# Performance work log

Hardware: AMD Instinct MI355X
Metric: run time of the kernel (lower is better)

The kernel has to match this reference:

```python
import jax, jax.numpy as jnp
import numpy as np

BIT_W = 8   # config.bit_wt
BIT_A = 8   # config.bit_act (activations sliced 2 bits at a time)
STRIDE = (1, 1)
PAD = 1


def _conv(a, w):
    # NCHW input, OIHW weight, stride 1, symmetric padding 1 (matches wrapped Conv2d)
    return jax.lax.conv_general_dilated(
        a, w, window_strides=STRIDE, padding=[(PAD, PAD), (PAD, PAD)],
        dimension_numbers=("NCHW", "OIHW", "NCHW"))


def setup_inputs() -> dict:
    key = jax.random.key(0)
    k1, k2, k3 = jax.random.split(key, 3)
    x = jax.random.normal(k1, (64, 64, 56, 56), dtype=jnp.float32)
    weight = jax.random.normal(k2, (64, 64, 3, 3), dtype=jnp.float32)
    bias = jax.random.normal(k3, (64,), dtype=jnp.float32)
    scale_a = jnp.full((1,), 20.0, dtype=jnp.float32)      # conv_q.scale
    scale_w = jnp.full((1,), 20.0, dtype=jnp.float32)      # wrapped_module.weight_scale
    zero_point = jnp.full((1,), -128.0, dtype=jnp.float32)  # conv_q.zero_point
    return {"x": x, "weight": weight, "bias": bias,
            "scale_a": scale_a, "scale_w": scale_w, "zero_point": zero_point}


def reference(x, weight, bias, scale_a, scale_w, zero_point):
    sa = scale_a[0]
    sw = scale_w[0]
    zp = zero_point[0]
    # activation quantization: round(x*scale_a - zero_point), clamp to [0, 2^bit_act - 1]
    q_in = jnp.clip(jnp.round(x * sa - zp), 0.0, 2.0 ** BIT_A - 1.0)
    # weight quantization: round(w * scale_w), interpreted in two's complement
    q_w = jnp.round(weight * sw)
    w_off = q_w + 2.0 ** BIT_W  # (w + (1 << bit_weight)) before bit masking

    acc = jnp.zeros((), dtype=jnp.float32)
    for ba in range(BIT_A // 2):
        # 2-bit activation slice: (a >> 2*ba) & 3
        a_sl = jnp.mod(jnp.floor(q_in / (4.0 ** ba)), 4.0)
        for bw in range(BIT_W):
            # weight bit bw: ((w + 2^B) >> bw) & 1
            w_bit = jnp.mod(jnp.floor(w_off / (2.0 ** bw)), 2.0)
            r = _conv(a_sl, w_bit)
            sgn = -1.0 if bw == BIT_W - 1 else 1.0  # MSB = sign bit (two's complement)
            acc = acc + sgn * (2.0 ** (2 * ba + bw)) * r

    # zero-point correction: conv(ones * zp, q_w) added back (no-op when zp == 0)
    acc = acc + zp * _conv(jnp.ones_like(q_in), q_w)

    out = acc / (sw * sa) + bias[None, :, None, None]
    return out
```

## Files before the change

### kernel.cpp

```cpp
#include <hip/hip_runtime.h>


typedef int v4i __attribute__((ext_vector_type(4)));
typedef float v4f __attribute__((ext_vector_type(4)));

__global__ __launch_bounds__(64) void prep_wq(const float* __restrict__ wt,
                                              const float* __restrict__ sw_p,
                                              const float* __restrict__ zp_p,
                                              signed char* __restrict__ w8,
                                              float* __restrict__ corr_tab) {
  const int o = blockIdx.x;
  const int i = threadIdx.x;
  const float sw = sw_p[0];
  const float* wp = wt + (size_t)(o * 64 + i) * 9;
  int q[9];
#pragma unroll
  for (int k = 0; k < 9; ++k) q[k] = (int)rintf(wp[k] * sw);
#pragma unroll
  for (int k = 0; k < 9; ++k)
    w8[(o * 9 + k) * 64 + i] = (signed char)(q[k] & 255);

  int stc[9], srw[9];
#pragma unroll
  for (int k = 0; k < 9; ++k) {
    int a = (int)(signed char)(q[k] & 255);
    int b = q[k];
#pragma unroll
    for (int off = 32; off; off >>= 1) {
      a += __shfl_xor(a, off);
      b += __shfl_xor(b, off);
    }
    stc[k] = a; srw[k] = b;
  }
  const float zp = zp_p[0];
  if (i < 9) {
    const int v = i / 3, hc = i % 3;
    float corr = 0.0f;
#pragma unroll
    for (int k = 0; k < 9; ++k) {
      const int kh = k / 3, kw = k % 3;
      const bool drop = (v == 1 && kh == 0) || (v == 2 && kh == 2) ||
                        (hc == 1 && kw == 0) || (hc == 2 && kw == 2);
      if (!drop) corr += 128.0f * (float)stc[k] + zp * (float)srw[k];
    }
    corr_tab[i * 64 + o] = corr;
  }
}

__global__ __launch_bounds__(256, 4) void conv_fused(
    const float* __restrict__ x, const signed char* __restrict__ w8,
    const float* __restrict__ corr_tab, const float* __restrict__ bias,
    const float* __restrict__ sa_p, const float* __restrict__ sw_p,
    const float* __restrict__ zp_p, float* __restrict__ out) {
  __shared__ __align__(16) signed char lds[22272];
  const int tid = threadIdx.x;
  const int b = blockIdx.x;
  const int g = (b & 7) * 112 + (b >> 3);
  const int n = (g * 2341) >> 15;
  const int h0 = (g - n * 14) * 4;
  const float sa = sa_p[0], zp = zp_p[0];
  const float* xim = x + (size_t)n * 200704;

#pragma unroll 2
  for (int it = 0; it < 6; ++it) {
    const int idx = tid + 256 * it;
    if (idx < 1344) {
      const int cg = idx & 15;
      const int rem = idx >> 4;
      const int row = (rem * 2341) >> 15;
      const int w4 = rem - row * 14;
      const int ih = h0 - 1 + row;
      const bool valid = (unsigned)ih < 56u;
      v4f v[4];
      if (valid) {
#pragma unroll
        for (int j = 0; j < 4; ++j)
          v[j] = *(const v4f*)(xim + (size_t)(cg * 4 + j) * 3136 + ih * 56 + w4 * 4);
      }
#pragma unroll
      for (int e = 0; e < 4; ++e) {
        int dw = 0;
        if (valid) {
#pragma unroll
          for (int j = 0; j < 4; ++j) {
            float tq;
            {
#pragma clang fp contract(off)
              tq = v[j][e] * sa - zp;
            }
            float qf = rintf(tq);
            qf = fminf(fmaxf(qf, 0.0f), 255.0f);
            const int bb = ((int)qf - 128) & 255;
            dw |= bb << (8 * j);
          }
        }
        const int c = w4 * 4 + 1 + e;
        const int t = (c >> 1) & 3;
        ((int*)lds)[(row * 58 + c) * 16 + (((cg >> 2) ^ t) << 2) + (cg & 3)] = dw;
      }
    } else {
      const int z = idx - 1344;
      const int loc = z >> 4, d = z & 15;
      const int row = loc >> 1, side = loc & 1;
      ((int*)lds)[(row * 58 + side * 57) * 16 + d] = 0;
    }
  }
  __syncthreads();

  const int lane = tid & 63;
  const int wv = tid >> 6;
  const int phalf = wv & 1;
  const int ogp = wv >> 1;
  const int ln = lane & 15;
  const int kg = lane >> 4;
  const int oa = ogp * 32 + ln;

  const signed char* wba = w8 + (size_t)oa * 576 + kg * 16;
  v4i Ba[9], Bb[9];
#pragma unroll
  for (int t = 0; t < 9; ++t) {
    Ba[t] = *(const v4i*)(wba + t * 64);
    Bb[t] = *(const v4i*)(wba + 9216 + t * 64);
  }

  const float sw = sw_p[0];
  const float rden = 1.0f / (sw * sa);
  const float boa = bias[oa], bob = bias[oa + 16];
  const float cFa = corr_tab[oa];
  const float cFb = corr_tab[oa + 16];
  float* const outa = out + (size_t)(n * 64 + oa) * 3136 + h0 * 56;
  float* const outb = outa + 16 * 3136;

#pragma unroll 1
  for (int t = 0; t < 7; ++t) {
    const int pb = phalf * 112 + t * 16;
    const int pa = pb + ln;
    const int hr = (pa * 9363) >> 19;
    const int wc = pa - hr * 56;
    int coff[3];
#pragma unroll
    for (int kw = 0; kw < 3; ++kw) {
      const int c = wc + kw;
      coff[kw] = c * 64 + ((kg ^ ((c >> 1) & 3)) << 4);
    }
    const signed char* rowb = lds + hr * 3712;
    v4i acca = {0, 0, 0, 0}, accb = {0, 0, 0, 0};
#pragma unroll
    for (int kh = 0; kh < 3; ++kh) {
#pragma unroll
      for (int kw = 0; kw < 3; ++kw) {
        const v4i A = *(const v4i*)(rowb + kh * 3712 + coff[kw]);
        acca = __builtin_amdgcn_mfma_i32_16x16x64_i8(A, Ba[kh * 3 + kw], acca, 0, 0, 0);
        accb = __builtin_amdgcn_mfma_i32_16x16x64_i8(A, Bb[kh * 3 + kw], accb, 0, 0, 0);
      }
    }
    const int pxb = pb + kg * 4;
    float ta[4], tb[4];
#pragma unroll
    for (int e = 0; e < 4; ++e) {
      const int px = pxb + e;
      const int hh = (px * 9363) >> 19;
      const int ww = px - hh * 56;
      const int hg = h0 + hh;
      float ca = cFa, cb = cFb;
      if ((hg == 0) | (hg == 55) | (ww == 0) | (ww == 55)) {
        const int vcase = (hg == 0) ? 1 : ((hg == 55) ? 2 : 0);
        const int hcase = (ww == 0) ? 1 : ((ww == 55) ? 2 : 0);
        const int cidx = (vcase * 3 + hcase) * 64;
        ca = corr_tab[cidx + oa];
        cb = corr_tab[cidx + oa + 16];
      }
      ta[e] = ((float)acca[e] + ca) * rden + boa;
      tb[e] = ((float)accb[e] + cb) * rden + bob;
    }
    *(float4*)(outa + pxb) = make_float4(ta[0], ta[1], ta[2], ta[3]);
    *(float4*)(outb + pxb) = make_float4(tb[0], tb[1], tb[2], tb[3]);
  }
}

extern "C" void kernel_launch(void* const* d_in, const int* in_sizes, int n_in,
                              void* d_out, int out_size, void* d_ws, size_t ws_size,
                              hipStream_t stream) {
  const float* x    = (const float*)d_in[0];
  const float* wt   = (const float*)d_in[1];
  const float* bias = (const float*)d_in[2];
  const float* sa   = (const float*)d_in[3];
  const float* sw   = (const float*)d_in[4];
  const float* zp   = (const float*)d_in[5];
  float* out = (float*)d_out;

  char* ws = (char*)d_ws;
  signed char* w8 = (signed char*)ws;
  float* corr_tab = (float*)(ws + 36864);

  prep_wq<<<64, 64, 0, stream>>>(wt, sw, zp, w8, corr_tab);
  conv_fused<<<896, 256, 0, stream>>>(x, w8, corr_tab, bias, sa, sw, zp, out);
}
```

Baseline: 131.4 us.

## Halve conv row tile to two rows and give each wave 16 channels

Each block now computes 2 output rows instead of 4, so the grid doubles to 1792 blocks and LDS shrinks to 14848 bytes. Each wave now owns 16 output channels across both rows rather than 32 channels over half the pixels, which halves the resident weight registers and MFMA accumulators. Launch bounds are raised to 8 blocks per SM. The aim is higher occupancy and a more even spread of blocks across CUs, at the cost of more halo rows re-read and quantized per output row.

```diff
diff --git a/kernel.cpp b/kernel.cpp
--- a/kernel.cpp
+++ b/kernel.cpp
@@ -47,24 +47,24 @@
   }
 }
 
-__global__ __launch_bounds__(256, 4) void conv_fused(
+__global__ __launch_bounds__(256, 8) void conv_fused(
     const float* __restrict__ x, const signed char* __restrict__ w8,
     const float* __restrict__ corr_tab, const float* __restrict__ bias,
     const float* __restrict__ sa_p, const float* __restrict__ sw_p,
     const float* __restrict__ zp_p, float* __restrict__ out) {
-  __shared__ __align__(16) signed char lds[22272];
+  __shared__ __align__(16) signed char lds[14848];
   const int tid = threadIdx.x;
   const int b = blockIdx.x;
-  const int g = (b & 7) * 112 + (b >> 3);
-  const int n = (g * 2341) >> 15;
-  const int h0 = (g - n * 14) * 4;
+  const int g = (b & 7) * 224 + (b >> 3);
+  const int n = (g * 2341) >> 16;
+  const int h0 = (g - n * 28) * 2;
   const float sa = sa_p[0], zp = zp_p[0];
   const float* xim = x + (size_t)n * 200704;
 
 #pragma unroll 2
-  for (int it = 0; it < 6; ++it) {
+  for (int it = 0; it < 4; ++it) {
     const int idx = tid + 256 * it;
-    if (idx < 1344) {
+    if (idx < 896) {
       const int cg = idx & 15;
       const int rem = idx >> 4;
       const int row = (rem * 2341) >> 15;
@@ -99,7 +99,7 @@
         ((int*)lds)[(row * 58 + c) * 16 + (((cg >> 2) ^ t) << 2) + (cg & 3)] = dw;
       }
     } else {
-      const int z = idx - 1344;
+      const int z = idx - 896;
       const int loc = z >> 4, d = z & 15;
       const int row = loc >> 1, side = loc & 1;
       ((int*)lds)[(row * 58 + side * 57) * 16 + d] = 0;
@@ -109,33 +109,26 @@
 
   const int lane = tid & 63;
   const int wv = tid >> 6;
-  const int phalf = wv & 1;
-  const int ogp = wv >> 1;
   const int ln = lane & 15;
   const int kg = lane >> 4;
-  const int oa = ogp * 32 + ln;
+  const int oa = wv * 16 + ln;
 
   const signed char* wba = w8 + (size_t)oa * 576 + kg * 16;
-  v4i Ba[9], Bb[9];
+  v4i Ba[9];
 #pragma unroll
-  for (int t = 0; t < 9; ++t) {
-    Ba[t] = *(const v4i*)(wba + t * 64);
-    Bb[t] = *(const v4i*)(wba + 9216 + t * 64);
-  }
+  for (int t = 0; t < 9; ++t) Ba[t] = *(const v4i*)(wba + t * 64);
 
   const float sw = sw_p[0];
   const float rden = 1.0f / (sw * sa);
-  const float boa = bias[oa], bob = bias[oa + 16];
+  const float boa = bias[oa];
   const float cFa = corr_tab[oa];
-  const float cFb = corr_tab[oa + 16];
   float* const outa = out + (size_t)(n * 64 + oa) * 3136 + h0 * 56;
-  float* const outb = outa + 16 * 3136;
 
 #pragma unroll 1
   for (int t = 0; t < 7; ++t) {
-    const int pb = phalf * 112 + t * 16;
+    const int pb = t * 16;
     const int pa = pb + ln;
-    const int hr = (pa * 9363) >> 19;
+    const int hr = pa >= 56;
     const int wc = pa - hr * 56;
     int coff[3];
 #pragma unroll
@@ -144,37 +137,32 @@
       coff[kw] = c * 64 + ((kg ^ ((c >> 1) & 3)) << 4);
     }
     const signed char* rowb = lds + hr * 3712;
-    v4i acca = {0, 0, 0, 0}, accb = {0, 0, 0, 0};
+    v4i acca = {0, 0, 0, 0};
 #pragma unroll
     for (int kh = 0; kh < 3; ++kh) {
 #pragma unroll
       for (int kw = 0; kw < 3; ++kw) {
         const v4i A = *(const v4i*)(rowb + kh * 3712 + coff[kw]);
         acca = __builtin_amdgcn_mfma_i32_16x16x64_i8(A, Ba[kh * 3 + kw], acca, 0, 0, 0);
-        accb = __builtin_amdgcn_mfma_i32_16x16x64_i8(A, Bb[kh * 3 + kw], accb, 0, 0, 0);
       }
     }
     const int pxb = pb + kg * 4;
-    float ta[4], tb[4];
+    float ta[4];
 #pragma unroll
     for (int e = 0; e < 4; ++e) {
       const int px = pxb + e;
-      const int hh = (px * 9363) >> 19;
+      const int hh = px >= 56;
       const int ww = px - hh * 56;
       const int hg = h0 + hh;
-      float ca = cFa, cb = cFb;
+      float ca = cFa;
       if ((hg == 0) | (hg == 55) | (ww == 0) | (ww == 55)) {
         const int vcase = (hg == 0) ? 1 : ((hg == 55) ? 2 : 0);
         const int hcase = (ww == 0) ? 1 : ((ww == 55) ? 2 : 0);
-        const int cidx = (vcase * 3 + hcase) * 64;
-        ca = corr_tab[cidx + oa];
-        cb = corr_tab[cidx + oa + 16];
+        ca = corr_tab[(vcase * 3 + hcase) * 64 + oa];
       }
       ta[e] = ((float)acca[e] + ca) * rden + boa;
-      tb[e] = ((float)accb[e] + cb) * rden + bob;
     }
     *(float4*)(outa + pxb) = make_float4(ta[0], ta[1], ta[2], ta[3]);
-    *(float4*)(outb + pxb) = make_float4(tb[0], tb[1], tb[2], tb[3]);
   }
 }
 
@@ -194,5 +182,5 @@
   float* corr_tab = (float*)(ws + 36864);
 
   prep_wq<<<64, 64, 0, stream>>>(wt, sw, zp, w8, corr_tab);
-  conv_fused<<<896, 256, 0, stream>>>(x, w8, corr_tab, bias, sa, sw, zp, out);
+  conv_fused<<<1792, 256, 0, stream>>>(x, w8, corr_tab, bias, sa, sw, zp, out);
 }
```

Result: slower. 138.3 us (+5.2%).

## Split activation quantization into a separate int8 pre-pass kernel

Applied to the files above, without the earlier changes.

Moves activation quantization out of the conv kernel into a standalone kernel that writes a padded, swizzled int8 activation image to workspace, including zeroed halo rows and columns. The conv kernel then just copies its tile of int8 rows into LDS and runs the MFMA loop. This removes redundant halo-row float loads and per-block quantization ALU work from the conv kernel. In exchange it adds an extra kernel launch and a round trip of the int8 tensor through global memory.

```diff
diff --git a/kernel.cpp b/kernel.cpp
--- a/kernel.cpp
+++ b/kernel.cpp
@@ -3,6 +3,9 @@
 
 typedef int v4i __attribute__((ext_vector_type(4)));
 typedef float v4f __attribute__((ext_vector_type(4)));
+
+#define QA_ROW 3712
+#define QA_IMG 215296
 
 __global__ __launch_bounds__(64) void prep_wq(const float* __restrict__ wt,
                                               const float* __restrict__ sw_p,
@@ -47,62 +50,81 @@
   }
 }
 
-__global__ __launch_bounds__(256, 4) void conv_fused(
-    const float* __restrict__ x, const signed char* __restrict__ w8,
+__global__ __launch_bounds__(256) void quant_a(const float* __restrict__ x,
+                                               const float* __restrict__ sa_p,
+                                               const float* __restrict__ zp_p,
+                                               signed char* __restrict__ qa) {
+  const int bx = blockIdx.x;
+  const int n = blockIdx.y;
+  const int tid = threadIdx.x;
+  const float sa = sa_p[0], zp = zp_p[0];
+  const float* xim = x + (size_t)n * 200704;
+  signed char* const qim = qa + (size_t)n * QA_IMG;
+
+#pragma unroll
+  for (int it = 0; it < 4; ++it) {
+    const int idx = tid + 256 * it;
+    if (idx < 896) {
+      const int cg = idx & 15;
+      const int rem = idx >> 4;
+      const int r = (rem * 2341) >> 15;
+      const int w4 = rem - r * 14;
+      const int ih = bx * 4 + r;
+      v4f v[4];
+#pragma unroll
+      for (int j = 0; j < 4; ++j)
+        v[j] = *(const v4f*)(xim + (size_t)(cg * 4 + j) * 3136 + ih * 56 + w4 * 4);
+#pragma unroll
+      for (int e = 0; e < 4; ++e) {
+        int dw = 0;
+#pragma unroll
+        for (int j = 0; j < 4; ++j) {
+          float tq;
+          {
+#pragma clang fp contract(off)
+            tq = v[j][e] * sa - zp;
+          }
+          float qf = rintf(tq);
+          qf = fminf(fmaxf(qf, 0.0f), 255.0f);
+          dw |= (((int)qf - 128) & 255) << (8 * j);
+        }
+        const int c = w4 * 4 + 1 + e;
+        const int t = (c >> 1) & 3;
+        *(int*)(qim + (ih + 1) * QA_ROW + c * 64 +
+                (((cg >> 2) ^ t) << 4) + ((cg & 3) << 2)) = dw;
+      }
+    } else {
+      const int z = idx - 896;
+      const int loc = z >> 4, d = z & 15;
+      const int r = loc >> 1, side = loc & 1;
+      *(int*)(qim + (bx * 4 + 1 + r) * QA_ROW + side * 57 * 64 + d * 4) = 0;
+    }
+  }
+  if (bx == 0 && tid < 232)
+    ((uint4*)qim)[tid] = make_uint4(0, 0, 0, 0);
+  if (bx == 13 && tid < 232)
+    ((uint4*)(qim + (size_t)57 * QA_ROW))[tid] = make_uint4(0, 0, 0, 0);
+}
+
+__global__ __launch_bounds__(256, 4) void conv_mfma(
+    const signed char* __restrict__ qa, const signed char* __restrict__ w8,
     const float* __restrict__ corr_tab, const float* __restrict__ bias,
     const float* __restrict__ sa_p, const float* __restrict__ sw_p,
-    const float* __restrict__ zp_p, float* __restrict__ out) {
+    float* __restrict__ out) {
   __shared__ __align__(16) signed char lds[22272];
   const int tid = threadIdx.x;
   const int b = blockIdx.x;
   const int g = (b & 7) * 112 + (b >> 3);
   const int n = (g * 2341) >> 15;
   const int h0 = (g - n * 14) * 4;
-  const float sa = sa_p[0], zp = zp_p[0];
-  const float* xim = x + (size_t)n * 200704;
-
-#pragma unroll 2
-  for (int it = 0; it < 6; ++it) {
-    const int idx = tid + 256 * it;
-    if (idx < 1344) {
-      const int cg = idx & 15;
-      const int rem = idx >> 4;
-      const int row = (rem * 2341) >> 15;
-      const int w4 = rem - row * 14;
-      const int ih = h0 - 1 + row;
-      const bool valid = (unsigned)ih < 56u;
-      v4f v[4];
-      if (valid) {
-#pragma unroll
-        for (int j = 0; j < 4; ++j)
-          v[j] = *(const v4f*)(xim + (size_t)(cg * 4 + j) * 3136 + ih * 56 + w4 * 4);
-      }
-#pragma unroll
-      for (int e = 0; e < 4; ++e) {
-        int dw = 0;
-        if (valid) {
-#pragma unroll
-          for (int j = 0; j < 4; ++j) {
-            float tq;
-            {
-#pragma clang fp contract(off)
-              tq = v[j][e] * sa - zp;
-            }
-            float qf = rintf(tq);
-            qf = fminf(fmaxf(qf, 0.0f), 255.0f);
-            const int bb = ((int)qf - 128) & 255;
-            dw |= bb << (8 * j);
-          }
-        }
-        const int c = w4 * 4 + 1 + e;
-        const int t = (c >> 1) & 3;
-        ((int*)lds)[(row * 58 + c) * 16 + (((cg >> 2) ^ t) << 2) + (cg & 3)] = dw;
-      }
-    } else {
-      const int z = idx - 1344;
-      const int loc = z >> 4, d = z & 15;
-      const int row = loc >> 1, side = loc & 1;
-      ((int*)lds)[(row * 58 + side * 57) * 16 + d] = 0;
+
+  {
+    const uint4* src = (const uint4*)(qa + (size_t)n * QA_IMG + (size_t)h0 * QA_ROW);
+    uint4* dst = (uint4*)lds;
+#pragma unroll
+    for (int it = 0; it < 6; ++it) {
+      const int idx = tid + it * 256;
+      if (idx < 1392) dst[idx] = src[idx];
     }
   }
   __syncthreads();
@@ -123,7 +145,7 @@
     Bb[t] = *(const v4i*)(wba + 9216 + t * 64);
   }
 
-  const float sw = sw_p[0];
+  const float sa = sa_p[0], sw = sw_p[0];
   const float rden = 1.0f / (sw * sa);
   const float boa = bias[oa], bob = bias[oa + 16];
   const float cFa = corr_tab[oa];
@@ -143,13 +165,13 @@
       const int c = wc + kw;
       coff[kw] = c * 64 + ((kg ^ ((c >> 1) & 3)) << 4);
     }
-    const signed char* rowb = lds + hr * 3712;
+    const signed char* rowb = lds + hr * QA_ROW;
     v4i acca = {0, 0, 0, 0}, accb = {0, 0, 0, 0};
 #pragma unroll
     for (int kh = 0; kh < 3; ++kh) {
 #pragma unroll
       for (int kw = 0; kw < 3; ++kw) {
-        const v4i A = *(const v4i*)(rowb + kh * 3712 + coff[kw]);
+        const v4i A = *(const v4i*)(rowb + kh * QA_ROW + coff[kw]);
         acca = __builtin_amdgcn_mfma_i32_16x16x64_i8(A, Ba[kh * 3 + kw], acca, 0, 0, 0);
         accb = __builtin_amdgcn_mfma_i32_16x16x64_i8(A, Bb[kh * 3 + kw], accb, 0, 0, 0);
       }
@@ -190,9 +212,11 @@
   float* out = (float*)d_out;
 
   char* ws = (char*)d_ws;
-  signed char* w8 = (signed char*)ws;
-  float* corr_tab = (float*)(ws + 36864);
+  signed char* qa = (signed char*)ws;
+  signed char* w8 = (signed char*)(ws + 13778944);
+  float* corr_tab = (float*)(ws + 13778944 + 36864);
 
   prep_wq<<<64, 64, 0, stream>>>(wt, sw, zp, w8, corr_tab);
-  conv_fused<<<896, 256, 0, stream>>>(x, w8, corr_tab, bias, sa, sw, zp, out);
-}
+  quant_a<<<dim3(14, 64), 256, 0, stream>>>(x, sa, zp, qa);
+  conv_mfma<<<896, 256, 0, stream>>>(qa, w8, corr_tab, bias, sa, sw, out);
+}
```

After: 128.3 us. 2.4% less time.
